# Kernel optimization log

Measured on AMD Instinct MI355X. Metric: run time of the kernel, lower is better.

## Reference

```python
import jax, jax.numpy as jnp
import numpy as np

N = 8192       # node_num
F_IN = 256     # src_feature
F_OUT = 128    # out_feature
NEG_SLOPE = 0.2  # standard GAT leakyrelu slope
MASK_VAL = -1e12


def setup_inputs() -> dict:
    key = jax.random.key(0)
    k1, k2, k3, k4, k5, k6 = jax.random.split(key, 6)
    x = jax.random.normal(k1, (N, F_IN), dtype=jnp.float32)
    adj = jax.random.randint(k2, (N, N), 0, 2, dtype=jnp.int32)  # 0/1 adjacency mask
    # xavier-uniform-like scales
    W = jax.random.normal(k3, (F_IN, F_OUT), dtype=jnp.float32) * np.float32(1.0 / np.sqrt(F_IN))
    a1 = jax.random.normal(k4, (F_OUT,), dtype=jnp.float32) * np.float32(0.1)  # att[:F_OUT]
    a2 = jax.random.normal(k5, (F_OUT,), dtype=jnp.float32) * np.float32(0.1)  # att[F_OUT:]
    bias = jax.random.normal(k6, (F_OUT,), dtype=jnp.float32) * np.float32(0.1)
    return {"x": x, "adj": adj, "W": W, "a1": a1, "a2": a2, "bias": bias}


def reference(x, adj, W, a1, a2, bias):
    # h = x @ W1  (src_h == dst_h for int src_dst_feature)
    h = x @ W  # [N, F_OUT]
    # e[i,j] = leakyrelu(att^T [h_i || h_j]) decomposed as (h@a1)_i + (h@a2)_j
    s_src = h @ a1  # [N]
    s_dst = h @ a2  # [N]
    e = jax.nn.leaky_relu(s_src[:, None] + s_dst[None, :], NEG_SLOPE)  # [N, N]
    masked = jnp.where(adj > 0, e, jnp.float32(MASK_VAL))
    attention = jax.nn.softmax(masked, axis=1)  # [N, N]
    # dropout in eval mode = identity; aggregate neighbor features
    out = attention @ h + bias  # [N, F_OUT]
    return out
```

## Files before the change

### kernel.cpp

```cpp
#include <hip/hip_runtime.h>
#include <cstdint>
#include <cstddef>

#define NN 8192
#define FIN 256
#define FOUT 128
#define SLOPE 0.2f
#define SHIFT 8.0f

typedef float f32x4 __attribute__((ext_vector_type(4)));
typedef __bf16 bf16x8 __attribute__((ext_vector_type(8)));
typedef int i32x4 __attribute__((ext_vector_type(4)));
typedef unsigned int u32x4 __attribute__((ext_vector_type(4)));

__device__ __forceinline__ unsigned short f2bf(float f) {
  return __builtin_bit_cast(unsigned short, (__bf16)f);
}

__device__ __forceinline__ void async_cp16(void* lds, const void* g) {
  __builtin_amdgcn_global_load_lds(
      (const __attribute__((address_space(1))) void*)g,
      (__attribute__((address_space(3))) void*)lds, 16, 0, 0);
}

__global__ __launch_bounds__(256, 4) void k_hw(const float* __restrict__ x,
                                               const float* __restrict__ W,
                                               const float* __restrict__ a1,
                                               const float* __restrict__ a2,
                                               unsigned short* __restrict__ ht,
                                               float* __restrict__ Etab,
                                               unsigned short* __restrict__ FbfF,
                                               unsigned short* __restrict__ FbfF2) {
  __shared__ float xs[8][256];
  __shared__ unsigned short tile[128][8];
  const int tid = threadIdx.x;
  const int rowbase = blockIdx.x * 8;

  #pragma unroll
  for (int it = 0; it < 2; ++it) {
    int fi = it * 1024 + tid * 4;
    int r = fi >> 8, k = fi & 255;
    *(f32x4*)&xs[r][k] = *(const f32x4*)(x + (size_t)(rowbase + r) * FIN + k);
  }
  __syncthreads();

  const int r = tid >> 5;
  const int cg = tid & 31;
  f32x4 acc = {0.f, 0.f, 0.f, 0.f};

  #pragma unroll 8
  for (int k = 0; k < FIN; ++k) {
    f32x4 wv = *(const f32x4*)(W + k * FOUT + cg * 4);
    float xv = xs[r][k];
    acc[0] += xv * wv[0];
    acc[1] += xv * wv[1];
    acc[2] += xv * wv[2];
    acc[3] += xv * wv[3];
  }

  #pragma unroll
  for (int c = 0; c < 4; ++c) tile[cg * 4 + c][r] = f2bf(acc[c]);

  f32x4 av1 = *(const f32x4*)(a1 + cg * 4);
  f32x4 av2 = *(const f32x4*)(a2 + cg * 4);
  float s1 = acc[0] * av1[0] + acc[1] * av1[1] + acc[2] * av1[2] + acc[3] * av1[3];
  float s2 = acc[0] * av2[0] + acc[1] * av2[1] + acc[2] * av2[2] + acc[3] * av2[3];
  #pragma unroll
  for (int off = 16; off > 0; off >>= 1) {
    s1 += __shfl_xor(s1, off, 64);
    s2 += __shfl_xor(s2, off, 64);
  }
  if (cg == 0) {
    const int row = rowbase + r;
    float c0 = s1 + SHIFT;
    float c = fmaxf(c0, SLOPE * c0);
    Etab[(size_t)row * 2]     = __expf(s1 - c);
    Etab[(size_t)row * 2 + 1] = __expf(SLOPE * s1 - c);
    FbfF[row]  = f2bf(__expf(s2));
    FbfF2[row] = f2bf(__expf(SLOPE * s2));
  }
  __syncthreads();

  if (tid < 128) {
    u32x4 v = *(const u32x4*)&tile[tid][0];
    *(u32x4*)(ht + (size_t)tid * NN + rowbase) = v;
  }
}

__global__ __launch_bounds__(512, 4) void k_gat(const int* __restrict__ adj,
                                                const unsigned short* __restrict__ ht,
                                                const float* __restrict__ Etab,
                                                const unsigned short* __restrict__ FbfF,
                                                const unsigned short* __restrict__ FbfF2,
                                                float* __restrict__ part,
                                                float* __restrict__ denp) {
  __shared__ unsigned short sH[2][128 * 64];
  __shared__ unsigned int sAp[2][128][2];
  __shared__ unsigned short sF[2][128];

  const int tid = threadIdx.x;
  const int wave = tid >> 6;
  const int lane = tid & 63;
  const int quad = lane >> 4;
  const int m = lane & 15;
  const int rowbase = (int)(blockIdx.x >> 3) * 128;
  const int colbase = (int)(blockIdx.x & 7) * 1024;
  const int CB = (int)(blockIdx.x & 7);
  const int row = rowbase + wave * 16 + m;

  bf16x8 pm, pinv, pones;
  #pragma unroll
  for (int jj = 0; jj < 8; ++jj) {
    pm[jj] = (__bf16)(float)m;
    pinv[jj] = (__bf16)0.03125f;
    pones[jj] = (__bf16)1.0f;
  }
  f32x4 z = {0.f, 0.f, 0.f, 0.f};
  f32x4 rp = __builtin_amdgcn_mfma_f32_16x16x32_bf16(pm, pinv, z, 0, 0, 0);
  f32x4 cp = __builtin_amdgcn_mfma_f32_16x16x32_bf16(pinv, pm, z, 0, 0, 0);
  int rowmap[4], colmap[4];
  #pragma unroll
  for (int r = 0; r < 4; ++r) {
    rowmap[r] = ((int)(rp[r] + 0.5f)) & 15;
    colmap[r] = ((int)(cp[r] + 0.5f)) & 15;
  }

  const float E  = Etab[(size_t)row * 2];
  const float E2 = Etab[(size_t)row * 2 + 1];

  f32x4 acc[8];
  #pragma unroll
  for (int t = 0; t < 8; ++t) acc[t] = z;
  f32x4 den = z;

  const int* adjRow = adj + (size_t)(rowbase + wave * 16) * NN + colbase + lane;
  int aregs[16];
  auto loadA = [&](int c) {
    #pragma unroll
    for (int r = 0; r < 16; ++r)
      aregs[r] = adjRow[(size_t)r * NN + c * 64];
  };
  auto packA = [&](int b) {
    #pragma unroll
    for (int r = 0; r < 16; ++r) {
      const unsigned long long mk = __ballot(aregs[r] != 0);
      if (lane == 0)
        *(unsigned long long*)&sAp[b][wave * 16 + r][0] = mk;
    }
  };

  const unsigned short* srcH[2];
  #pragma unroll
  for (int il = 0; il < 2; ++il) {
    const int i = wave * 2 + il;
    const int f = i * 8 + (lane >> 3);
    const int g = (lane & 7) ^ (lane >> 3);
    srcH[il] = ht + (size_t)f * NN + colbase + g * 8;
  }
  const unsigned short* srcF = nullptr;
  if (wave == 1) {
    srcF = (lane < 8) ? (FbfF + colbase + lane * 8)
                      : (FbfF2 + colbase + (lane - 8) * 8);
  }

  auto stage = [&](int b, int c) {
    #pragma unroll
    for (int il = 0; il < 2; ++il)
      async_cp16(&sH[b][(wave * 2 + il) * 512], srcH[il] + c * 64);
    if (wave == 1 && lane < 16) async_cp16(&sF[b][0], srcF + c * 64);
  };

  auto compute = [&](int cs) {
    #pragma unroll
    for (int k32 = 0; k32 < 2; ++k32) {
      const unsigned int word = sAp[cs][wave * 16 + m][k32];
      const unsigned int byt = (word >> (quad * 8)) & 0xffu;
      const int jl = k32 * 32 + quad * 8;
      u32x4 Fq = *(const u32x4*)&sF[cs][jl];
      u32x4 Gq = *(const u32x4*)&sF[cs][64 + jl];

      bf16x8 af;
      #pragma unroll
      for (int p = 0; p < 4; ++p) {
        const unsigned fp = Fq[p], gp = Gq[p];
        const float Flo = __builtin_bit_cast(float, fp << 16);
        const float Fhi = __builtin_bit_cast(float, fp & 0xffff0000u);
        const float Glo = __builtin_bit_cast(float, gp << 16);
        const float Ghi = __builtin_bit_cast(float, gp & 0xffff0000u);
        const float wlo = fmaxf(E * Flo, E2 * Glo);
        const float whi = fmaxf(E * Fhi, E2 * Ghi);
        af[p * 2]     = (byt & (1u << (p * 2)))     ? (__bf16)wlo : (__bf16)0.0f;
        af[p * 2 + 1] = (byt & (1u << (p * 2 + 1))) ? (__bf16)whi : (__bf16)0.0f;
      }

      const int s0 = (k32 * 4 + quad) ^ (m & 7);
      #pragma unroll
      for (int t = 0; t < 8; ++t) {
        bf16x8 bt = __builtin_bit_cast(bf16x8,
            *(const u32x4*)&sH[cs][(t * 16 + m) * 64 + s0 * 8]);
        acc[t] = __builtin_amdgcn_mfma_f32_16x16x32_bf16(af, bt, acc[t], 0, 0, 0);
      }
      den = __builtin_amdgcn_mfma_f32_16x16x32_bf16(af, pones, den, 0, 0, 0);
    }
  };

  loadA(0);
  packA(0);
  loadA(1);
  stage(0, 0);

  #pragma unroll 1
  for (int c = 0; c < 16; ++c) {
    const int cs = c & 1, ns = cs ^ 1;
    __syncthreads();
    if (c + 1 < 16) {
      packA(ns);
      loadA(c + 2 < 16 ? c + 2 : 15);
      stage(ns, c + 1);
    }
    compute(cs);
  }

  float* sOut = (float*)&sH[0][0];
  #pragma unroll
  for (int h = 0; h < 2; ++h) {
    __syncthreads();
    #pragma unroll
    for (int r = 0; r < 4; ++r) {
      #pragma unroll
      for (int tt = 0; tt < 4; ++tt) {
        sOut[(wave * 16 + rowmap[r]) * 64 + tt * 16 + colmap[r]] =
            acc[h * 4 + tt][r];
      }
    }
    __syncthreads();
    #pragma unroll
    for (int i = 0; i < 4; ++i) {
      const int v = i * 512 + tid;
      const int rl = v >> 4, c4 = v & 15;
      *(f32x4*)&part[((size_t)CB * NN + rowbase + rl) * FOUT + h * 64 + c4 * 4] =
          ((const f32x4*)sOut)[v];
    }
  }
  if (m == 0) {
    #pragma unroll
    for (int r = 0; r < 4; ++r)
      denp[(size_t)CB * NN + rowbase + wave * 16 + rowmap[r]] = den[r];
  }
}

__global__ __launch_bounds__(256) void k_fin(const float* __restrict__ part,
                                             const float* __restrict__ denp,
                                             const float* __restrict__ bias,
                                             float* __restrict__ out) {
  const int i4 = blockIdx.x * 256 + threadIdx.x;
  const int rowi = i4 >> 5;
  const int f = (i4 & 31) * 4;
  float den = 0.f;
  f32x4 s = {0.f, 0.f, 0.f, 0.f};
  #pragma unroll
  for (int cb = 0; cb < 8; ++cb) {
    den += denp[(size_t)cb * NN + rowi];
    f32x4 p = *(const f32x4*)&part[((size_t)cb * NN + rowi) * FOUT + f];
    s[0] += p[0]; s[1] += p[1]; s[2] += p[2]; s[3] += p[3];
  }
  const float inv = 1.0f / den;
  f32x4 b = *(const f32x4*)(bias + f);
  f32x4 v = {s[0] * inv + b[0], s[1] * inv + b[1],
             s[2] * inv + b[2], s[3] * inv + b[3]};
  *(f32x4*)(out + (size_t)rowi * FOUT + f) = v;
}

extern "C" void kernel_launch(void* const* d_in, const int* in_sizes, int n_in,
                              void* d_out, int out_size, void* d_ws, size_t ws_size,
                              hipStream_t stream) {
  const float* x    = (const float*)d_in[0];
  const int*   adj  = (const int*)d_in[1];
  const float* W    = (const float*)d_in[2];
  const float* a1   = (const float*)d_in[3];
  const float* a2   = (const float*)d_in[4];
  const float* bias = (const float*)d_in[5];
  float* out = (float*)d_out;

  char* ws = (char*)d_ws;
  unsigned short* ht = (unsigned short*)ws;
  float* Etab = (float*)(ws + (size_t)2 * 1024 * 1024);
  unsigned short* FbfF =
      (unsigned short*)(ws + (size_t)2 * 1024 * 1024 + 64 * 1024);
  unsigned short* FbfF2 = FbfF + NN;
  float* part = (float*)(ws + (size_t)4 * 1024 * 1024);
  float* denp = (float*)(ws + (size_t)36 * 1024 * 1024);

  k_hw<<<NN / 8, 256, 0, stream>>>(x, W, a1, a2, ht, Etab, FbfF, FbfF2);
  k_gat<<<512, 512, 0, stream>>>(adj, ht, Etab, FbfF, FbfF2, part, denp);
  k_fin<<<(NN * FOUT / 4) / 256, 256, 0, stream>>>(part, denp, bias, out);
}
```

Before: 443.2 us.

## Load F/G coefficients into registers and hand-tune waitcnt pipeline with setprio

Drops the LDS staging of the per-column F/G exponent factors. Each lane now loads them straight from global memory into registers per chunk. The generic __syncthreads is replaced with raw s_barrier plus explicit partial vmcnt/lgkmcnt waits, so the adjacency and H prefetches for later chunks stay in flight while the current chunk computes. s_setprio raises wave priority during the MFMA compute phase. The hard-coded vmcnt counts depend on the exact number of outstanding loads, so any change in issue order could break correctness.

```diff
diff --git a/kernel.cpp b/kernel.cpp
--- a/kernel.cpp
+++ b/kernel.cpp
@@ -96,7 +96,6 @@
                                                 float* __restrict__ denp) {
   __shared__ unsigned short sH[2][128 * 64];
   __shared__ unsigned int sAp[2][128][2];
-  __shared__ unsigned short sF[2][128];
 
   const int tid = threadIdx.x;
   const int wave = tid >> 6;
@@ -149,6 +148,16 @@
     }
   };
 
+  const unsigned short* fbase = FbfF  + colbase + quad * 8;
+  const unsigned short* gbase = FbfF2 + colbase + quad * 8;
+  u32x4 F0, F1, G0, G1;
+  auto loadF = [&](int c) {
+    F0 = *(const u32x4*)(fbase + c * 64);
+    F1 = *(const u32x4*)(fbase + c * 64 + 32);
+    G0 = *(const u32x4*)(gbase + c * 64);
+    G1 = *(const u32x4*)(gbase + c * 64 + 32);
+  };
+
   const unsigned short* srcH[2];
   #pragma unroll
   for (int il = 0; il < 2; ++il) {
@@ -157,17 +166,10 @@
     const int g = (lane & 7) ^ (lane >> 3);
     srcH[il] = ht + (size_t)f * NN + colbase + g * 8;
   }
-  const unsigned short* srcF = nullptr;
-  if (wave == 1) {
-    srcF = (lane < 8) ? (FbfF + colbase + lane * 8)
-                      : (FbfF2 + colbase + (lane - 8) * 8);
-  }
-
   auto stage = [&](int b, int c) {
     #pragma unroll
     for (int il = 0; il < 2; ++il)
       async_cp16(&sH[b][(wave * 2 + il) * 512], srcH[il] + c * 64);
-    if (wave == 1 && lane < 16) async_cp16(&sF[b][0], srcF + c * 64);
   };
 
   auto compute = [&](int cs) {
@@ -175,9 +177,8 @@
     for (int k32 = 0; k32 < 2; ++k32) {
       const unsigned int word = sAp[cs][wave * 16 + m][k32];
       const unsigned int byt = (word >> (quad * 8)) & 0xffu;
-      const int jl = k32 * 32 + quad * 8;
-      u32x4 Fq = *(const u32x4*)&sF[cs][jl];
-      u32x4 Gq = *(const u32x4*)&sF[cs][64 + jl];
+      const u32x4 Fq = k32 ? F1 : F0;
+      const u32x4 Gq = k32 ? G1 : G0;
 
       bf16x8 af;
       #pragma unroll
@@ -205,6 +206,7 @@
   };
 
   loadA(0);
+  asm volatile("s_waitcnt vmcnt(0)" ::: "memory");
   packA(0);
   loadA(1);
   stage(0, 0);
@@ -212,13 +214,22 @@
   #pragma unroll 1
   for (int c = 0; c < 16; ++c) {
     const int cs = c & 1, ns = cs ^ 1;
-    __syncthreads();
-    if (c + 1 < 16) {
+    if (c > 0) __builtin_amdgcn_s_barrier();
+    if (c < 15) {
+      asm volatile("s_waitcnt vmcnt(2)" ::: "memory");
       packA(ns);
+      loadF(c);
       loadA(c + 2 < 16 ? c + 2 : 15);
       stage(ns, c + 1);
-    }
+      asm volatile("s_waitcnt vmcnt(18) lgkmcnt(0)" ::: "memory");
+    } else {
+      loadF(15);
+      asm volatile("s_waitcnt vmcnt(0) lgkmcnt(0)" ::: "memory");
+    }
+    __builtin_amdgcn_s_barrier();
+    __builtin_amdgcn_s_setprio(1);
     compute(cs);
+    __builtin_amdgcn_s_setprio(0);
   }
 
   float* sOut = (float*)&sH[0][0];
```

New measurement: 445.1 us. About the same (+0.4%).
